# Performance work log

Hardware: AMD Instinct MI355X
Metric: run time of the kernel (lower is better)

## Reference

```python
import jax, jax.numpy as jnp
import numpy as np

NUM_HEADS = 16
TOP_K = 128
LN_EPS = 1e-5


def layernorm(x, w, b):
    mu = jnp.mean(x, axis=-1, keepdims=True)
    var = jnp.mean((x - mu) ** 2, axis=-1, keepdims=True)
    return (x - mu) * jax.lax.rsqrt(var + LN_EPS) * w + b


def top_k_activation(x, k):
    # keep top-k along last dim, zero elsewhere (scatter, like torch.scatter_)
    n = x.shape[-1]
    if k >= n:
        return x
    vals, idx = jax.lax.top_k(x, k)
    flat = x.reshape(-1, n)
    rows = jnp.arange(flat.shape[0])[:, None]
    out = jnp.zeros_like(flat).at[rows, idx.reshape(-1, k)].set(vals.reshape(-1, k))
    return out.reshape(x.shape)


def setup_inputs() -> dict:
    key = jax.random.key(0)
    ks = jax.random.split(key, 8)
    B, S, H = 2, 2048, 1024
    hd = H // NUM_HEADS
    return {
        "x": jax.random.normal(ks[0], (B, S, H), dtype=jnp.float32),
        "W_Q": jax.random.normal(ks[1], (H, H), dtype=jnp.float32) * 0.02,
        "W_K": jax.random.normal(ks[2], (H, H), dtype=jnp.float32) * 0.02,
        "W_V": jax.random.normal(ks[3], (H, H), dtype=jnp.float32) * 0.02,
        "W_O": jax.random.normal(ks[4], (H, H), dtype=jnp.float32) * 0.02,
        "q_ln_w": jnp.ones((hd,), dtype=jnp.float32),
        "q_ln_b": jnp.zeros((hd,), dtype=jnp.float32),
        "k_ln_w": jnp.ones((hd,), dtype=jnp.float32),
        "k_ln_b": jnp.zeros((hd,), dtype=jnp.float32),
        "sparse_W_V": jax.random.normal(ks[5], (NUM_HEADS, hd, TOP_K), dtype=jnp.float32) * 0.02,
        "sparse_W_O": jax.random.normal(ks[6], (NUM_HEADS, TOP_K, hd), dtype=jnp.float32) * 0.02,
    }


def reference(x, W_Q, W_K, W_V, W_O, q_ln_w, q_ln_b, k_ln_w, k_ln_b, sparse_W_V, sparse_W_O):
    B, S, H = x.shape
    nh = sparse_W_V.shape[0]
    hd = H // nh
    # projections (torch Linear: x @ W.T)
    def split_heads(t):
        return t.reshape(B, S, nh, hd).transpose(0, 2, 1, 3)  # [B, nh, S, hd]
    Q = split_heads(jnp.einsum('bsd,od->bso', x, W_Q))
    K = split_heads(jnp.einsum('bsd,od->bso', x, W_K))
    V = split_heads(jnp.einsum('bsd,od->bso', x, W_V))
    Q = layernorm(Q, q_ln_w, q_ln_b)
    K = layernorm(K, k_ln_w, k_ln_b)
    scores = jnp.einsum('bhqd,bhkd->bhqk', Q, K) / jnp.sqrt(jnp.float32(hd))
    attn = jax.nn.softmax(scores, axis=-1)
    context = jnp.einsum('bhqk,bhkd->bhqd', attn, V)  # [B, nh, S, hd]
    # faithful to source: transpose then reshape mixes batch/seq/head dims
    context_flat = context.transpose(0, 2, 1, 3).reshape(B * nh, S, hd)
    v_weights = sparse_W_V.mean(axis=2)  # [nh, hd]
    z = jnp.einsum('bnd,hd->bhn', context_flat, v_weights)  # [B*nh, nh, S]
    z_sparse = top_k_activation(z, TOP_K)  # top-k along seq axis, as in source
    o_weights = sparse_W_O.mean(axis=1)  # [nh, hd]
    y_flat = jnp.einsum('bhn,hd->bnd', z_sparse, o_weights)  # [B*nh, S, hd]
    y = y_flat.reshape(B, nh, S, hd).transpose(0, 2, 1, 3).reshape(B, S, H)
    y = jnp.einsum('bsd,od->bso', y, W_O)
    return y
```

## Files before the change

### kernel.cpp

```cpp
#include <hip/hip_runtime.h>
#include <math.h>

#define NB   2
#define SEQ  2048
#define NHD  16
#define HDD  64
#define HID  1024
#define TOPK 128

__global__ void k_prep_means(const float* __restrict__ sWV, const float* __restrict__ sWO,
                             double* __restrict__ vw, double* __restrict__ ow) {
  int t = threadIdx.x;
  for (int o = t; o < NHD * HDD; o += 256) {
    const float* p = sWV + (size_t)o * TOPK;
    double s = 0.0;
    for (int i = 0; i < TOPK; i++) s += (double)p[i];
    vw[o] = s * (1.0 / 128.0);
    int h = o >> 6, d = o & 63;
    const float* q = sWO + ((size_t)h * TOPK) * HDD + d;
    double s2 = 0.0;
    for (int i = 0; i < TOPK; i++) s2 += (double)q[(size_t)i * HDD];
    ow[o] = s2 * (1.0 / 128.0);
  }
}

__global__ void k_prep_wvp_g(const float* __restrict__ W_V, const float* __restrict__ W_O,
                             const double* __restrict__ vw, const double* __restrict__ ow,
                             double* __restrict__ WVP, float* __restrict__ G) {
  int blk = blockIdx.x;
  int t = threadIdx.x;
  if (blk < 256) {
    int n = blk >> 4, h = blk & 15;
    for (int j = t; j < HID; j += 256) {
      double s = 0.0;
      for (int d = 0; d < 64; d++)
        s += (double)W_V[(size_t)(n * 64 + d) * HID + j] * vw[h * 64 + d];
      WVP[(size_t)blk * HID + j] = s;
    }
  } else {
    int r = blk - 256;
    int m = r >> 4, h = r & 15;
    for (int o = t; o < HID; o += 256) {
      double s = 0.0;
      for (int d = 0; d < 64; d++)
        s += ow[h * 64 + d] * (double)W_O[(size_t)o * HID + m * 64 + d];
      G[(size_t)r * HID + o] = (float)s;
    }
  }
}

__global__ __launch_bounds__(256) void k_proj_qk(
    const float* __restrict__ x, const float* __restrict__ W_Q, const float* __restrict__ W_K,
    const float* __restrict__ qw, const float* __restrict__ qb,
    const float* __restrict__ kw, const float* __restrict__ kb,
    double* __restrict__ Qh, double* __restrict__ Kh) {
  __shared__ float  As[64][33];
  __shared__ float  Bs[64][33];
  __shared__ double Cs[64][65];
  __shared__ double red[64][4];

  int rt = blockIdx.x, ot = blockIdx.y;
  bool isQ = (ot < 16);
  const float* W = isQ ? W_Q : W_K;
  int head = isQ ? ot : ot - 16;
  int o0 = head * 64;
  int t = threadIdx.x;
  int tr = t >> 4, tc = t & 15;

  double acc[4][4];
  #pragma unroll
  for (int i = 0; i < 4; i++)
    #pragma unroll
    for (int j = 0; j < 4; j++) acc[i][j] = 0.0;

  for (int k0 = 0; k0 < HID; k0 += 32) {
    #pragma unroll
    for (int i = 0; i < 8; i++) {
      int idx = t + i * 256;
      int r = idx >> 5, c = idx & 31;
      As[r][c] = x[(size_t)(rt * 64 + r) * HID + k0 + c];
      Bs[r][c] = W[(size_t)(o0 + r) * HID + k0 + c];
    }
    __syncthreads();
    #pragma unroll 1
    for (int kk = 0; kk < 32; kk++) {
      double a[4], b[4];
      #pragma unroll
      for (int i = 0; i < 4; i++) a[i] = (double)As[tr * 4 + i][kk];
      #pragma unroll
      for (int j = 0; j < 4; j++) b[j] = (double)Bs[tc * 4 + j][kk];
      #pragma unroll
      for (int i = 0; i < 4; i++)
        #pragma unroll
        for (int j = 0; j < 4; j++) acc[i][j] = fma(a[i], b[j], acc[i][j]);
    }
    __syncthreads();
  }

  #pragma unroll
  for (int i = 0; i < 4; i++)
    #pragma unroll
    for (int j = 0; j < 4; j++) Cs[tr * 4 + i][tc * 4 + j] = acc[i][j];
  __syncthreads();

  int r = t >> 2, p = t & 3;
  double s = 0.0;
  for (int i = 0; i < 16; i++) s += Cs[r][p * 16 + i];
  red[r][p] = s;
  __syncthreads();
  double mu = (red[r][0] + red[r][1] + red[r][2] + red[r][3]) * (1.0 / 64.0);
  __syncthreads();
  double s2 = 0.0;
  for (int i = 0; i < 16; i++) { double dl = Cs[r][p * 16 + i] - mu; s2 += dl * dl; }
  red[r][p] = s2;
  __syncthreads();
  double var = (red[r][0] + red[r][1] + red[r][2] + red[r][3]) * (1.0 / 64.0);
  double inv = 1.0 / sqrt(var + 1e-5);

  int R = rt * 64 + r;
  int b = R >> 11, ss = R & 2047;
  const float* lw = isQ ? qw : kw;
  const float* lb = isQ ? qb : kb;
  double* outp = isQ ? Qh : Kh;
  size_t base = (((size_t)b * 16 + head) * SEQ + ss) * 64;
  for (int i = 0; i < 16; i++) {
    int d = p * 16 + i;
    outp[base + d] = (Cs[r][d] - mu) * inv * (double)lw[d] + (double)lb[d];
  }
}

__global__ __launch_bounds__(256) void k_proj_vp(
    const float* __restrict__ x, const double* __restrict__ WVP, double* __restrict__ Vp) {
  __shared__ float  As[64][33];
  __shared__ double Bs[64][33];
  int rt = blockIdx.x, ot = blockIdx.y;
  int t = threadIdx.x, tr = t >> 4, tc = t & 15;

  double acc[4][4];
  #pragma unroll
  for (int i = 0; i < 4; i++)
    #pragma unroll
    for (int j = 0; j < 4; j++) acc[i][j] = 0.0;

  for (int k0 = 0; k0 < HID; k0 += 32) {
    #pragma unroll
    for (int i = 0; i < 8; i++) {
      int idx = t + i * 256;
      int r = idx >> 5, c = idx & 31;
      As[r][c] = x[(size_t)(rt * 64 + r) * HID + k0 + c];
      Bs[r][c] = WVP[(size_t)(ot * 64 + r) * HID + k0 + c];
    }
    __syncthreads();
    #pragma unroll 1
    for (int kk = 0; kk < 32; kk++) {
      double a[4], b[4];
      #pragma unroll
      for (int i = 0; i < 4; i++) a[i] = (double)As[tr * 4 + i][kk];
      #pragma unroll
      for (int j = 0; j < 4; j++) b[j] = Bs[tc * 4 + j][kk];
      #pragma unroll
      for (int i = 0; i < 4; i++)
        #pragma unroll
        for (int j = 0; j < 4; j++) acc[i][j] = fma(a[i], b[j], acc[i][j]);
    }
    __syncthreads();
  }
  #pragma unroll
  for (int i = 0; i < 4; i++) {
    int R = rt * 64 + tr * 4 + i;
    int b = R >> 11, k = R & 2047;
    #pragma unroll
    for (int j = 0; j < 4; j++) {
      int cc = ot * 64 + tc * 4 + j;
      int n = cc >> 4, h = cc & 15;
      Vp[((((size_t)b * 16 + n) * SEQ) + k) * 16 + h] = acc[i][j];
    }
  }
}

__global__ __launch_bounds__(256, 2) void k_attn(
    const double* __restrict__ Qh, const double* __restrict__ Kh,
    const double* __restrict__ Vp, double* __restrict__ pnum, double* __restrict__ pden) {
  int kh = blockIdx.x;
  int qt = blockIdx.y;
  int bn = blockIdx.z;
  int t = threadIdx.x;
  int s = qt * 256 + t;

  __shared__ double Klds[64][64];
  __shared__ double Vplds[64][16];

  double qd[64];
  const double* qp = Qh + ((size_t)bn * SEQ + s) * 64;
  #pragma unroll
  for (int d = 0; d < 64; d++) qd[d] = qp[d];

  double num[16];
  #pragma unroll
  for (int h = 0; h < 16; h++) num[h] = 0.0;
  double den = 0.0;

  int k0 = kh * 1024;
  for (int kc = 0; kc < 1024; kc += 64) {
    const double* kbase = Kh + ((size_t)bn * SEQ + k0 + kc) * 64;
    #pragma unroll
    for (int i = 0; i < 16; i++) {
      int idx = t + i * 256;
      Klds[idx >> 6][idx & 63] = kbase[idx];
    }
    const double* vbase = Vp + ((size_t)bn * SEQ + k0 + kc) * 16;
    #pragma unroll
    for (int i = 0; i < 4; i++) {
      int idx = t + i * 256;
      Vplds[idx >> 4][idx & 15] = vbase[idx];
    }
    __syncthreads();
    #pragma unroll 1
    for (int kk = 0; kk < 64; kk += 4) {
      double s0 = 0.0, s1 = 0.0, s2 = 0.0, s3 = 0.0;
      #pragma unroll
      for (int d = 0; d < 64; d++) {
        double q = qd[d];
        s0 = fma(q, Klds[kk + 0][d], s0);
        s1 = fma(q, Klds[kk + 1][d], s1);
        s2 = fma(q, Klds[kk + 2][d], s2);
        s3 = fma(q, Klds[kk + 3][d], s3);
      }
      double e0 = exp(s0 * 0.125);
      double e1 = exp(s1 * 0.125);
      double e2 = exp(s2 * 0.125);
      double e3 = exp(s3 * 0.125);
      den += (e0 + e1) + (e2 + e3);
      #pragma unroll
      for (int h = 0; h < 16; h++) {
        double a = num[h];
        a = fma(e0, Vplds[kk + 0][h], a);
        a = fma(e1, Vplds[kk + 1][h], a);
        a = fma(e2, Vplds[kk + 2][h], a);
        a = fma(e3, Vplds[kk + 3][h], a);
        num[h] = a;
      }
    }
    __syncthreads();
  }
  size_t pb = ((size_t)kh * 32 + bn) * SEQ + s;
  pden[pb] = den;
  #pragma unroll
  for (int h = 0; h < 16; h++) pnum[pb * 16 + h] = num[h];
}

__global__ void k_combine(const double* __restrict__ pnum, const double* __restrict__ pden,
                          double* __restrict__ zrow) {
  int id = blockIdx.x * 256 + threadIdx.x;
  int bn = id >> 11, s = id & 2047;
  int b = bn >> 4, n = bn & 15;
  double den = pden[id] + pden[65536 + id];
  int bp = b * 16 + (s >> 7);
  int np = ((s & 127) << 4) | n;
  size_t p0 = (size_t)id * 16, p1 = ((size_t)65536 + id) * 16;
  for (int h = 0; h < 16; h++) {
    double nm = pnum[p0 + h] + pnum[p1 + h];
    zrow[((size_t)bp * 16 + h) * 2048 + np] = nm / den;
  }
}

__device__ inline unsigned long long dkey(double v) {
  unsigned long long u = (unsigned long long)__double_as_longlong(v);
  return (u & 0x8000000000000000ULL) ? ~u : (u | 0x8000000000000000ULL);
}

__global__ __launch_bounds__(256) void k_topk(const double* __restrict__ zrow,
                                              float* __restrict__ zs) {
  int row = blockIdx.x;
  int t = threadIdx.x;
  const double* src = zrow + (size_t)row * 2048;
  double v[8];
  unsigned long long key[8];
  #pragma unroll
  for (int i = 0; i < 8; i++) { v[i] = src[t + i * 256]; key[i] = dkey(v[i]); }

  __shared__ unsigned sh_cnt[4];
  __shared__ unsigned sh_cg[4], sh_ce[4];
  int w = t >> 6, lane = t & 63;

  unsigned long long lo = 0ULL, hi = 0xFFFFFFFFFFFFFFFFULL;
  while (lo < hi) {
    unsigned long long mid = lo + ((hi - lo) >> 1);
    unsigned c = 0;
    #pragma unroll
    for (int i = 0; i < 8; i++) c += (key[i] > mid) ? 1u : 0u;
    for (int off = 32; off; off >>= 1) c += __shfl_down(c, off);
    if (lane == 0) sh_cnt[w] = c;
    __syncthreads();
    unsigned total = sh_cnt[0] + sh_cnt[1] + sh_cnt[2] + sh_cnt[3];
    __syncthreads();
    if (total < TOPK) hi = mid; else lo = mid + 1;
  }
  unsigned long long tau = lo;

  unsigned cg = 0, ce = 0;
  #pragma unroll
  for (int i = 0; i < 8; i++) {
    cg += (key[i] > tau) ? 1u : 0u;
    ce += (key[i] == tau) ? 1u : 0u;
  }
  for (int off = 32; off; off >>= 1) { cg += __shfl_down(cg, off); ce += __shfl_down(ce, off); }
  if (lane == 0) { sh_cg[w] = cg; sh_ce[w] = ce; }
  __syncthreads();
  unsigned c_gt = sh_cg[0] + sh_cg[1] + sh_cg[2] + sh_cg[3];
  unsigned c_eq = sh_ce[0] + sh_ce[1] + sh_ce[2] + sh_ce[3];
  unsigned need = TOPK - c_gt;

  unsigned idxThr = 2048;
  if (c_eq > need) {
    unsigned l2 = 0, h2 = 2048;
    while (l2 < h2) {
      unsigned m2 = (l2 + h2) >> 1;
      unsigned c = 0;
      #pragma unroll
      for (int i = 0; i < 8; i++) {
        unsigned idx = (unsigned)(t + i * 256);
        c += (key[i] == tau && idx < m2) ? 1u : 0u;
      }
      for (int off = 32; off; off >>= 1) c += __shfl_down(c, off);
      if (lane == 0) sh_cnt[w] = c;
      __syncthreads();
      unsigned tot = sh_cnt[0] + sh_cnt[1] + sh_cnt[2] + sh_cnt[3];
      __syncthreads();
      if (tot >= need) h2 = m2; else l2 = m2 + 1;
    }
    idxThr = l2;
  }

  float* dst = zs + (size_t)row * 2048;
  #pragma unroll
  for (int i = 0; i < 8; i++) {
    unsigned idx = (unsigned)(t + i * 256);
    bool keep = (key[i] > tau) ||
                (key[i] == tau && (c_eq <= need || idx < idxThr));
    dst[idx] = keep ? (float)v[i] : 0.0f;
  }
}

__global__ __launch_bounds__(256) void k_out(const float* __restrict__ zs,
                                             const float* __restrict__ G,
                                             float* __restrict__ out) {
  __shared__ float Al[64][65];
  __shared__ float Bl[64][65];
  int rt = blockIdx.x, ot = blockIdx.y;
  int t = threadIdx.x, tr = t >> 4, tc = t & 15;
  int Rb = rt * 64;
  int b = Rb >> 11, s0 = Rb & 2047;

  float acc[4][4];
  #pragma unroll
  for (int i = 0; i < 4; i++)
    #pragma unroll
    for (int j = 0; j < 4; j++) acc[i][j] = 0.0f;

  for (int kc = 0; kc < 256; kc += 64) {
    #pragma unroll
    for (int i = 0; i < 16; i++) {
      int idx = t + i * 256;
      int c = idx >> 6, r = idx & 63;
      int cc = kc + c;
      Al[r][c] = zs[(((size_t)(b * 16 + (cc >> 4))) * 16 + (cc & 15)) * 2048 + s0 + r];
      Bl[c][r] = G[(size_t)(kc + c) * HID + ot * 64 + r];
    }
    __syncthreads();
    #pragma unroll 1
    for (int kk = 0; kk < 64; kk++) {
      float a[4], bb[4];
      #pragma unroll
      for (int i = 0; i < 4; i++) a[i] = Al[tr * 4 + i][kk];
      #pragma unroll
      for (int j = 0; j < 4; j++) bb[j] = Bl[kk][tc * 4 + j];
      #pragma unroll
      for (int i = 0; i < 4; i++)
        #pragma unroll
        for (int j = 0; j < 4; j++) acc[i][j] = fmaf(a[i], bb[j], acc[i][j]);
    }
    __syncthreads();
  }
  #pragma unroll
  for (int i = 0; i < 4; i++) {
    int R = Rb + tr * 4 + i;
    #pragma unroll
    for (int j = 0; j < 4; j++)
      out[(size_t)R * HID + ot * 64 + tc * 4 + j] = acc[i][j];
  }
}

extern "C" void kernel_launch(void* const* d_in, const int* in_sizes, int n_in,
                              void* d_out, int out_size, void* d_ws, size_t ws_size,
                              hipStream_t stream) {
  const float* x   = (const float*)d_in[0];
  const float* W_Q = (const float*)d_in[1];
  const float* W_K = (const float*)d_in[2];
  const float* W_V = (const float*)d_in[3];
  const float* W_O = (const float*)d_in[4];
  const float* qw  = (const float*)d_in[5];
  const float* qb  = (const float*)d_in[6];
  const float* kw  = (const float*)d_in[7];
  const float* kb  = (const float*)d_in[8];
  const float* sWV = (const float*)d_in[9];
  const float* sWO = (const float*)d_in[10];
  float* out = (float*)d_out;
  char* ws = (char*)d_ws;

  double* Qh   = (double*)(ws + 0);
  double* Kh   = (double*)(ws + 33554432ULL);
  double* Vp   = (double*)(ws + 67108864ULL);
  double* WVP  = (double*)(ws + 75497472ULL);
  float*  G    = (float*) (ws + 77594624ULL);
  double* vw   = (double*)(ws + 78643200ULL);
  double* ow   = (double*)(ws + 78651392ULL);
  double* pnum = (double*)(ws + 78659584ULL);
  double* pden = (double*)(ws + 95436800ULL);
  double* zrow = (double*)(ws + 0);
  float*  zs   = (float*) (ws + 8388608ULL);

  k_prep_means<<<dim3(1), dim3(256), 0, stream>>>(sWV, sWO, vw, ow);
  k_prep_wvp_g<<<dim3(512), dim3(256), 0, stream>>>(W_V, W_O, vw, ow, WVP, G);
  k_proj_qk<<<dim3(64, 32), dim3(256), 0, stream>>>(x, W_Q, W_K, qw, qb, kw, kb, Qh, Kh);
  k_proj_vp<<<dim3(64, 4), dim3(256), 0, stream>>>(x, WVP, Vp);
  k_attn<<<dim3(2, 8, 32), dim3(256), 0, stream>>>(Qh, Kh, Vp, pnum, pden);
  k_combine<<<dim3(256), dim3(256), 0, stream>>>(pnum, pden, zrow);
  k_topk<<<dim3(512), dim3(256), 0, stream>>>(zrow, zs);
  k_out<<<dim3(64, 16), dim3(256), 0, stream>>>(zs, G, out);
}
```

Before: 1.615 ms.

## Restructure projection GEMMs, register LayerNorm, split attention rows across thread pairs, fast exp

The projection kernels now store double-precision transposed tiles in LDS and read them as double2 vectors, and the QK LayerNorm is computed from register accumulators with wavefront shuffles instead of a shared staging tile. The attention kernel splits each query's head dimension across two threads, which halves per-thread registers and doubles the grid, and it raises the occupancy hint. A custom polynomial exp replaces the library exp. This aims to cut register pressure, LDS traffic and transcendental cost, but the polynomial exp may differ slightly from the library exp in accuracy and has no overflow handling.

```diff
diff --git a/kernel.cpp b/kernel.cpp
--- a/kernel.cpp
+++ b/kernel.cpp
@@ -7,6 +7,27 @@
 #define HDD  64
 #define HID  1024
 #define TOPK 128
+
+__device__ inline double fast_exp_s8(double s) {
+  const double C = 0.125 * 1.4426950408889634073599246810019;
+  double t = s * C;
+  double n = __builtin_rint(t);
+  double f = t - n;
+  double r = f * 0.69314718055994530941723212145818;
+  double p = 2.7557319223985890652557319223986e-6;
+  p = fma(p, r, 2.4801587301587301587301587301587e-5);
+  p = fma(p, r, 1.9841269841269841269841269841270e-4);
+  p = fma(p, r, 1.3888888888888888888888888888889e-3);
+  p = fma(p, r, 8.3333333333333333333333333333333e-3);
+  p = fma(p, r, 4.1666666666666666666666666666667e-2);
+  p = fma(p, r, 1.6666666666666666666666666666667e-1);
+  p = fma(p, r, 0.5);
+  p = fma(p, r, 1.0);
+  p = fma(p, r, 1.0);
+  int ni = (int)n;
+  double sc = __longlong_as_double((long long)(1023 + ni) << 52);
+  return p * sc;
+}
 
 __global__ void k_prep_means(const float* __restrict__ sWV, const float* __restrict__ sWO,
                              double* __restrict__ vw, double* __restrict__ ow) {
@@ -49,21 +70,18 @@
   }
 }
 
-__global__ __launch_bounds__(256) void k_proj_qk(
+__global__ __launch_bounds__(256, 4) void k_proj_qk(
     const float* __restrict__ x, const float* __restrict__ W_Q, const float* __restrict__ W_K,
     const float* __restrict__ qw, const float* __restrict__ qb,
     const float* __restrict__ kw, const float* __restrict__ kb,
     double* __restrict__ Qh, double* __restrict__ Kh) {
-  __shared__ float  As[64][33];
-  __shared__ float  Bs[64][33];
-  __shared__ double Cs[64][65];
-  __shared__ double red[64][4];
+  __shared__ __align__(16) double As[32][68];
+  __shared__ __align__(16) double Bs[32][68];
 
   int rt = blockIdx.x, ot = blockIdx.y;
   bool isQ = (ot < 16);
   const float* W = isQ ? W_Q : W_K;
   int head = isQ ? ot : ot - 16;
-  int o0 = head * 64;
   int t = threadIdx.x;
   int tr = t >> 4, tc = t & 15;
 
@@ -78,61 +96,73 @@
     for (int i = 0; i < 8; i++) {
       int idx = t + i * 256;
       int r = idx >> 5, c = idx & 31;
-      As[r][c] = x[(size_t)(rt * 64 + r) * HID + k0 + c];
-      Bs[r][c] = W[(size_t)(o0 + r) * HID + k0 + c];
-    }
-    __syncthreads();
-    #pragma unroll 1
+      As[c][r] = (double)x[(size_t)(rt * 64 + r) * HID + k0 + c];
+      Bs[c][r] = (double)W[(size_t)(head * 64 + r) * HID + k0 + c];
+    }
+    __syncthreads();
+    #pragma unroll 2
     for (int kk = 0; kk < 32; kk++) {
-      double a[4], b[4];
-      #pragma unroll
-      for (int i = 0; i < 4; i++) a[i] = (double)As[tr * 4 + i][kk];
-      #pragma unroll
-      for (int j = 0; j < 4; j++) b[j] = (double)Bs[tc * 4 + j][kk];
-      #pragma unroll
-      for (int i = 0; i < 4; i++)
-        #pragma unroll
-        for (int j = 0; j < 4; j++) acc[i][j] = fma(a[i], b[j], acc[i][j]);
-    }
-    __syncthreads();
-  }
-
-  #pragma unroll
-  for (int i = 0; i < 4; i++)
-    #pragma unroll
-    for (int j = 0; j < 4; j++) Cs[tr * 4 + i][tc * 4 + j] = acc[i][j];
-  __syncthreads();
-
-  int r = t >> 2, p = t & 3;
-  double s = 0.0;
-  for (int i = 0; i < 16; i++) s += Cs[r][p * 16 + i];
-  red[r][p] = s;
-  __syncthreads();
-  double mu = (red[r][0] + red[r][1] + red[r][2] + red[r][3]) * (1.0 / 64.0);
-  __syncthreads();
-  double s2 = 0.0;
-  for (int i = 0; i < 16; i++) { double dl = Cs[r][p * 16 + i] - mu; s2 += dl * dl; }
-  red[r][p] = s2;
-  __syncthreads();
-  double var = (red[r][0] + red[r][1] + red[r][2] + red[r][3]) * (1.0 / 64.0);
-  double inv = 1.0 / sqrt(var + 1e-5);
-
-  int R = rt * 64 + r;
-  int b = R >> 11, ss = R & 2047;
-  const float* lw = isQ ? qw : kw;
-  const float* lb = isQ ? qb : kb;
+      double2 a01 = *(const double2*)&As[kk][tr * 4];
+      double2 a23 = *(const double2*)&As[kk][tr * 4 + 2];
+      double2 b01 = *(const double2*)&Bs[kk][tc * 4];
+      double2 b23 = *(const double2*)&Bs[kk][tc * 4 + 2];
+      acc[0][0] = fma(a01.x, b01.x, acc[0][0]);
+      acc[0][1] = fma(a01.x, b01.y, acc[0][1]);
+      acc[0][2] = fma(a01.x, b23.x, acc[0][2]);
+      acc[0][3] = fma(a01.x, b23.y, acc[0][3]);
+      acc[1][0] = fma(a01.y, b01.x, acc[1][0]);
+      acc[1][1] = fma(a01.y, b01.y, acc[1][1]);
+      acc[1][2] = fma(a01.y, b23.x, acc[1][2]);
+      acc[1][3] = fma(a01.y, b23.y, acc[1][3]);
+      acc[2][0] = fma(a23.x, b01.x, acc[2][0]);
+      acc[2][1] = fma(a23.x, b01.y, acc[2][1]);
+      acc[2][2] = fma(a23.x, b23.x, acc[2][2]);
+      acc[2][3] = fma(a23.x, b23.y, acc[2][3]);
+      acc[3][0] = fma(a23.y, b01.x, acc[3][0]);
+      acc[3][1] = fma(a23.y, b01.y, acc[3][1]);
+      acc[3][2] = fma(a23.y, b23.x, acc[3][2]);
+      acc[3][3] = fma(a23.y, b23.y, acc[3][3]);
+    }
+    __syncthreads();
+  }
+
+  double lw[4], lb2[4];
+  {
+    const float* lwp = isQ ? qw : kw;
+    const float* lbp = isQ ? qb : kb;
+    #pragma unroll
+    for (int j = 0; j < 4; j++) {
+      lw[j]  = (double)lwp[tc * 4 + j];
+      lb2[j] = (double)lbp[tc * 4 + j];
+    }
+  }
   double* outp = isQ ? Qh : Kh;
-  size_t base = (((size_t)b * 16 + head) * SEQ + ss) * 64;
-  for (int i = 0; i < 16; i++) {
-    int d = p * 16 + i;
-    outp[base + d] = (Cs[r][d] - mu) * inv * (double)lw[d] + (double)lb[d];
-  }
-}
-
-__global__ __launch_bounds__(256) void k_proj_vp(
+  #pragma unroll
+  for (int i = 0; i < 4; i++) {
+    double s = (acc[i][0] + acc[i][1]) + (acc[i][2] + acc[i][3]);
+    s += __shfl_xor(s, 1); s += __shfl_xor(s, 2);
+    s += __shfl_xor(s, 4); s += __shfl_xor(s, 8);
+    double mu = s * (1.0 / 64.0);
+    double d0 = acc[i][0] - mu, d1 = acc[i][1] - mu;
+    double d2 = acc[i][2] - mu, d3 = acc[i][3] - mu;
+    double v = (d0 * d0 + d1 * d1) + (d2 * d2 + d3 * d3);
+    v += __shfl_xor(v, 1); v += __shfl_xor(v, 2);
+    v += __shfl_xor(v, 4); v += __shfl_xor(v, 8);
+    double inv = 1.0 / sqrt(v * (1.0 / 64.0) + 1e-5);
+    int R = rt * 64 + tr * 4 + i;
+    int b = R >> 11, ss = R & 2047;
+    double* op = outp + (((size_t)b * 16 + head) * SEQ + ss) * 64 + tc * 4;
+    op[0] = fma(d0 * inv, lw[0], lb2[0]);
+    op[1] = fma(d1 * inv, lw[1], lb2[1]);
+    op[2] = fma(d2 * inv, lw[2], lb2[2]);
+    op[3] = fma(d3 * inv, lw[3], lb2[3]);
+  }
+}
+
+__global__ __launch_bounds__(256, 4) void k_proj_vp(
     const float* __restrict__ x, const double* __restrict__ WVP, double* __restrict__ Vp) {
-  __shared__ float  As[64][33];
-  __shared__ double Bs[64][33];
+  __shared__ __align__(16) double As[32][68];
+  __shared__ __align__(16) double Bs[32][68];
   int rt = blockIdx.x, ot = blockIdx.y;
   int t = threadIdx.x, tr = t >> 4, tc = t & 15;
 
@@ -147,21 +177,32 @@
     for (int i = 0; i < 8; i++) {
       int idx = t + i * 256;
       int r = idx >> 5, c = idx & 31;
-      As[r][c] = x[(size_t)(rt * 64 + r) * HID + k0 + c];
-      Bs[r][c] = WVP[(size_t)(ot * 64 + r) * HID + k0 + c];
-    }
-    __syncthreads();
-    #pragma unroll 1
+      As[c][r] = (double)x[(size_t)(rt * 64 + r) * HID + k0 + c];
+      Bs[c][r] = WVP[(size_t)(ot * 64 + r) * HID + k0 + c];
+    }
+    __syncthreads();
+    #pragma unroll 2
     for (int kk = 0; kk < 32; kk++) {
-      double a[4], b[4];
-      #pragma unroll
-      for (int i = 0; i < 4; i++) a[i] = (double)As[tr * 4 + i][kk];
-      #pragma unroll
-      for (int j = 0; j < 4; j++) b[j] = Bs[tc * 4 + j][kk];
-      #pragma unroll
-      for (int i = 0; i < 4; i++)
-        #pragma unroll
-        for (int j = 0; j < 4; j++) acc[i][j] = fma(a[i], b[j], acc[i][j]);
+      double2 a01 = *(const double2*)&As[kk][tr * 4];
+      double2 a23 = *(const double2*)&As[kk][tr * 4 + 2];
+      double2 b01 = *(const double2*)&Bs[kk][tc * 4];
+      double2 b23 = *(const double2*)&Bs[kk][tc * 4 + 2];
+      acc[0][0] = fma(a01.x, b01.x, acc[0][0]);
+      acc[0][1] = fma(a01.x, b01.y, acc[0][1]);
+      acc[0][2] = fma(a01.x, b23.x, acc[0][2]);
+      acc[0][3] = fma(a01.x, b23.y, acc[0][3]);
+      acc[1][0] = fma(a01.y, b01.x, acc[1][0]);
+      acc[1][1] = fma(a01.y, b01.y, acc[1][1]);
+      acc[1][2] = fma(a01.y, b23.x, acc[1][2]);
+      acc[1][3] = fma(a01.y, b23.y, acc[1][3]);
+      acc[2][0] = fma(a23.x, b01.x, acc[2][0]);
+      acc[2][1] = fma(a23.x, b01.y, acc[2][1]);
+      acc[2][2] = fma(a23.x, b23.x, acc[2][2]);
+      acc[2][3] = fma(a23.x, b23.y, acc[2][3]);
+      acc[3][0] = fma(a23.y, b01.x, acc[3][0]);
+      acc[3][1] = fma(a23.y, b01.y, acc[3][1]);
+      acc[3][2] = fma(a23.y, b23.x, acc[3][2]);
+      acc[3][3] = fma(a23.y, b23.y, acc[3][3]);
     }
     __syncthreads();
   }
@@ -169,84 +210,90 @@
   for (int i = 0; i < 4; i++) {
     int R = rt * 64 + tr * 4 + i;
     int b = R >> 11, k = R & 2047;
-    #pragma unroll
-    for (int j = 0; j < 4; j++) {
-      int cc = ot * 64 + tc * 4 + j;
-      int n = cc >> 4, h = cc & 15;
-      Vp[((((size_t)b * 16 + n) * SEQ) + k) * 16 + h] = acc[i][j];
-    }
-  }
-}
-
-__global__ __launch_bounds__(256, 2) void k_attn(
+    int cc = ot * 64 + tc * 4;
+    int n = cc >> 4, h = cc & 15;
+    double* op = Vp + (((size_t)b * 16 + n) * SEQ + k) * 16 + h;
+    op[0] = acc[i][0]; op[1] = acc[i][1]; op[2] = acc[i][2]; op[3] = acc[i][3];
+  }
+}
+
+__global__ __launch_bounds__(256, 4) void k_attn(
     const double* __restrict__ Qh, const double* __restrict__ Kh,
     const double* __restrict__ Vp, double* __restrict__ pnum, double* __restrict__ pden) {
   int kh = blockIdx.x;
   int qt = blockIdx.y;
   int bn = blockIdx.z;
   int t = threadIdx.x;
-  int s = qt * 256 + t;
-
-  __shared__ double Klds[64][64];
-  __shared__ double Vplds[64][16];
-
-  double qd[64];
-  const double* qp = Qh + ((size_t)bn * SEQ + s) * 64;
-  #pragma unroll
-  for (int d = 0; d < 64; d++) qd[d] = qp[d];
-
-  double num[16];
-  #pragma unroll
-  for (int h = 0; h < 16; h++) num[h] = 0.0;
+  int q = qt * 128 + (t >> 1);
+  int half = t & 1;
+
+  __shared__ double2 Klds2[2048];
+  __shared__ double2 Vplds2[512];
+
+  double2 qd2[16];
+  const double2* qp2 = (const double2*)(Qh + ((size_t)bn * SEQ + q) * 64 + half * 32);
+  #pragma unroll
+  for (int i = 0; i < 16; i++) qd2[i] = qp2[i];
+
+  double num[8];
+  #pragma unroll
+  for (int j = 0; j < 8; j++) num[j] = 0.0;
   double den = 0.0;
 
   int k0 = kh * 1024;
   for (int kc = 0; kc < 1024; kc += 64) {
-    const double* kbase = Kh + ((size_t)bn * SEQ + k0 + kc) * 64;
-    #pragma unroll
-    for (int i = 0; i < 16; i++) {
-      int idx = t + i * 256;
-      Klds[idx >> 6][idx & 63] = kbase[idx];
-    }
-    const double* vbase = Vp + ((size_t)bn * SEQ + k0 + kc) * 16;
-    #pragma unroll
-    for (int i = 0; i < 4; i++) {
-      int idx = t + i * 256;
-      Vplds[idx >> 4][idx & 15] = vbase[idx];
-    }
+    const double2* kb2 = (const double2*)(Kh + ((size_t)bn * SEQ + k0 + kc) * 64);
+    #pragma unroll
+    for (int i = 0; i < 8; i++) Klds2[t + i * 256] = kb2[t + i * 256];
+    const double2* vb2 = (const double2*)(Vp + ((size_t)bn * SEQ + k0 + kc) * 16);
+    #pragma unroll
+    for (int i = 0; i < 2; i++) Vplds2[t + i * 256] = vb2[t + i * 256];
     __syncthreads();
     #pragma unroll 1
-    for (int kk = 0; kk < 64; kk += 4) {
-      double s0 = 0.0, s1 = 0.0, s2 = 0.0, s3 = 0.0;
-      #pragma unroll
-      for (int d = 0; d < 64; d++) {
-        double q = qd[d];
-        s0 = fma(q, Klds[kk + 0][d], s0);
-        s1 = fma(q, Klds[kk + 1][d], s1);
-        s2 = fma(q, Klds[kk + 2][d], s2);
-        s3 = fma(q, Klds[kk + 3][d], s3);
+    for (int kk = 0; kk < 64; kk += 2) {
+      const double2* kr2 = Klds2 + kk * 32 + half * 16;
+      double s0 = 0.0, s1 = 0.0;
+      #pragma unroll
+      for (int i = 0; i < 16; i++) {
+        double2 kv0 = kr2[i];
+        double2 kv1 = kr2[32 + i];
+        double2 qv = qd2[i];
+        s0 = fma(qv.x, kv0.x, s0);
+        s0 = fma(qv.y, kv0.y, s0);
+        s1 = fma(qv.x, kv1.x, s1);
+        s1 = fma(qv.y, kv1.y, s1);
       }
-      double e0 = exp(s0 * 0.125);
-      double e1 = exp(s1 * 0.125);
-      double e2 = exp(s2 * 0.125);
-      double e3 = exp(s3 * 0.125);
-      den += (e0 + e1) + (e2 + e3);
-      #pragma unroll
-      for (int h = 0; h < 16; h++) {
-        double a = num[h];
-        a = fma(e0, Vplds[kk + 0][h], a);
-        a = fma(e1, Vplds[kk + 1][h], a);
-        a = fma(e2, Vplds[kk + 2][h], a);
-        a = fma(e3, Vplds[kk + 3][h], a);
-        num[h] = a;
+      s0 += __shfl_xor(s0, 1);
+      s1 += __shfl_xor(s1, 1);
+      double xm = half ? s1 : s0;
+      double em = fast_exp_s8(xm);
+      double eo = __shfl_xor(em, 1);
+      double e0 = half ? eo : em;
+      double e1 = half ? em : eo;
+      den += e0 + e1;
+      const double2* vr2 = Vplds2 + kk * 8 + half * 4;
+      #pragma unroll
+      for (int j = 0; j < 4; j++) {
+        double2 v0 = vr2[j];
+        double2 v1 = vr2[8 + j];
+        double a0 = num[2 * j], a1 = num[2 * j + 1];
+        a0 = fma(e0, v0.x, a0);
+        a1 = fma(e0, v0.y, a1);
+        a0 = fma(e1, v1.x, a0);
+        a1 = fma(e1, v1.y, a1);
+        num[2 * j] = a0; num[2 * j + 1] = a1;
       }
     }
     __syncthreads();
   }
-  size_t pb = ((size_t)kh * 32 + bn) * SEQ + s;
-  pden[pb] = den;
-  #pragma unroll
-  for (int h = 0; h < 16; h++) pnum[pb * 16 + h] = num[h];
+  size_t pb = ((size_t)kh * 32 + bn) * SEQ + q;
+  if (half == 0) pden[pb] = den;
+  double2* pn2 = (double2*)(pnum + pb * 16 + half * 8);
+  #pragma unroll
+  for (int j = 0; j < 4; j++) {
+    double2 w2; w2.x = num[2 * j]; w2.y = num[2 * j + 1];
+    pn2[j] = w2;
+  }
 }
 
 __global__ void k_combine(const double* __restrict__ pnum, const double* __restrict__ pden,
@@ -424,7 +471,7 @@
   k_prep_wvp_g<<<dim3(512), dim3(256), 0, stream>>>(W_V, W_O, vw, ow, WVP, G);
   k_proj_qk<<<dim3(64, 32), dim3(256), 0, stream>>>(x, W_Q, W_K, qw, qb, kw, kb, Qh, Kh);
   k_proj_vp<<<dim3(64, 4), dim3(256), 0, stream>>>(x, WVP, Vp);
-  k_attn<<<dim3(2, 8, 32), dim3(256), 0, stream>>>(Qh, Kh, Vp, pnum, pden);
+  k_attn<<<dim3(2, 16, 32), dim3(256), 0, stream>>>(Qh, Kh, Vp, pnum, pden);
   k_combine<<<dim3(256), dim3(256), 0, stream>>>(pnum, pden, zrow);
   k_topk<<<dim3(512), dim3(256), 0, stream>>>(zrow, zs);
   k_out<<<dim3(64, 16), dim3(256), 0, stream>>>(zs, G, out);
```

New measurement: 1.969 ms. 1.22x slower.
